# Kernel optimization log

Hardware: AMD Instinct MI355X
Metric: run time of the kernel (lower is better)

## Reference

```python
import jax, jax.numpy as jnp
import numpy as np

B, T, C, H = 256, 256, 384, 64
MAX_REL = 3  # max_relative_position hardcoded in module


def setup_inputs() -> dict:
    key = jax.random.key(0)
    ks = jax.random.split(key, 6)
    s = 1.0 / np.sqrt(C)
    return {
        "x": jax.random.normal(ks[0], (B, T, C), dtype=jnp.float32),
        "Wq": jax.random.normal(ks[1], (C, H), dtype=jnp.float32) * s,
        "Wk": jax.random.normal(ks[2], (C, H), dtype=jnp.float32) * s,
        "Wv": jax.random.normal(ks[3], (C, H), dtype=jnp.float32) * s,
        "rel_k_table": jax.random.normal(ks[4], (2 * MAX_REL + 1, H), dtype=jnp.float32) * s,
        "rel_v_table": jax.random.normal(ks[5], (2 * MAX_REL + 1, H), dtype=jnp.float32) * s,
    }


def reference(x, Wq, Wk, Wv, rel_k_table, rel_v_table):
    Bd, Td, Cd = x.shape
    Hd = Wq.shape[1]
    q = x @ Wq  # [B,T,H]
    k = x @ Wk
    v = x @ Wv
    # relative position indices, clipped Shaw-style
    r = jnp.arange(Td)
    idx = jnp.clip(r[None, :] - r[:, None], -MAX_REL, MAX_REL) + MAX_REL  # [T,T]
    rk = rel_k_table[idx]  # [T,T,H]
    rv = rel_v_table[idx]  # [T,T,H]
    attn1 = jnp.einsum('bth,bsh->bts', q, k)
    attn2 = jnp.einsum('bth,tsh->bts', q, rk)
    scale = jnp.sqrt(jnp.asarray(Hd, dtype=x.dtype))
    scores = (attn1 + attn2) / scale
    causal = jnp.tril(jnp.ones((Td, Td), dtype=bool))
    scores = jnp.where(causal[None, :, :], scores, -jnp.inf)
    attn = jax.nn.softmax(scores, axis=-1)  # dropout = identity (eval mode)
    w1 = jnp.einsum('bts,bsh->bth', attn, v)
    w2 = jnp.einsum('bts,tsh->bth', attn, rv)
    return w1 + w2  # [B,T,H]
```

## Files before the change

### kernel.cpp

```cpp
#include <hip/hip_runtime.h>
#include <hip/hip_bf16.h>


typedef __attribute__((ext_vector_type(8))) __bf16 bf16x8;
typedef __attribute__((ext_vector_type(8))) short short8;
typedef __attribute__((ext_vector_type(4))) float f32x4;
typedef __attribute__((ext_vector_type(4))) int   i32x4;

#define MFMA16(A, B, C) __builtin_amdgcn_mfma_f32_16x16x32_bf16((A), (B), (C), 0, 0, 0)

__device__ __forceinline__ unsigned short f2bf(float f) {
    unsigned int u = __builtin_bit_cast(unsigned int, f);
    u = (u + 0x7FFFu + ((u >> 16) & 1u)) >> 16;
    return (unsigned short)u;
}
__device__ __forceinline__ float bf2f(unsigned short s) {
    unsigned int u = ((unsigned int)s) << 16;
    return __builtin_bit_cast(float, u);
}
__device__ __forceinline__ bf16x8 ld16(const unsigned short* p) {
    return __builtin_bit_cast(bf16x8, *(const i32x4*)p);
}

__global__ void prep_wt(const float* __restrict__ Wq, const float* __restrict__ Wk,
                        const float* __restrict__ Wv, const float* __restrict__ relk,
                        unsigned short* __restrict__ Wt, unsigned short* __restrict__ Rk) {
    int i = blockIdx.x * 256 + threadIdx.x;
    if (i < 3 * 64 * 384) {
        int kk = i % 384;
        int h  = (i / 384) & 63;
        int w  = i / (384 * 64);
        const float* W = (w == 0) ? Wq : ((w == 1) ? Wk : Wv);
        Wt[i] = f2bf(W[kk * 64 + h]);
    } else if (i < 3 * 64 * 384 + 1024) {
        int j = i - 3 * 64 * 384;
        int n = j >> 6, h = j & 63;
        Rk[j] = (n < 4) ? f2bf(relk[n * 64 + h]) : (unsigned short)0;
    }
}

__global__ __launch_bounds__(1024)
__attribute__((amdgpu_waves_per_eu(4, 4)))
void fused_kernel(
        const float* __restrict__ x, const unsigned short* __restrict__ Wt,
        const unsigned short* __restrict__ Rk, const float* __restrict__ relv,
        float* __restrict__ out) {
    extern __shared__ unsigned short sh[];
    unsigned short* ws  = sh;
    unsigned short* ksh = sh;
    unsigned short* vTs = sh + 18432;
    unsigned short* qs  = sh + 35328;
    float* lsum = (float*)(sh + 69120);

    const int tid  = threadIdx.x;
    const int wave = tid >> 6;
    const int lane = tid & 63;
    const int c    = lane & 15;
    const int quad = lane >> 4;
    const int b    = blockIdx.x;

    const f32x4 zero = {0.f, 0.f, 0.f, 0.f};

    const float* xbase = x + (size_t)(b * 256 + wave * 16 + c) * 384 + quad * 8;

    f32x4 aq[4], ak[4], av[4];
#pragma unroll
    for (int nt = 0; nt < 4; nt++) { aq[nt] = zero; ak[nt] = zero; av[nt] = zero; }

    f32x4 tmp[8];
#pragma unroll
    for (int j = 0; j < 4; j++) {
        tmp[2 * j]     = *(const f32x4*)(xbase + j * 32);
        tmp[2 * j + 1] = *(const f32x4*)(xbase + j * 32 + 4);
    }

#pragma unroll
    for (int it = 0; it < 9; it++) {
        int P_ = it * 1024 + tid;
        int r = P_ / 48, pc = P_ % 48;
        i32x4 d = *(const i32x4*)(Wt + r * 384 + pc * 8);
        *(i32x4*)(ws + r * 392 + pc * 8) = d;
    }
    __syncthreads();

#pragma unroll
    for (int ck = 0; ck < 3; ck++) {
        bf16x8 a[4];
#pragma unroll
        for (int j = 0; j < 4; j++) {
            short8 xs8;
#pragma unroll
            for (int e = 0; e < 4; e++) {
                xs8[e]     = (short)f2bf(tmp[2 * j][e]);
                xs8[4 + e] = (short)f2bf(tmp[2 * j + 1][e]);
            }
            a[j] = __builtin_bit_cast(bf16x8, xs8);
        }
        if (ck < 2) {
#pragma unroll
            for (int j = 0; j < 4; j++) {
                const float* xp = xbase + (ck + 1) * 128 + j * 32;
                tmp[2 * j]     = *(const f32x4*)xp;
                tmp[2 * j + 1] = *(const f32x4*)(xp + 4);
            }
        }

#pragma unroll
        for (int j = 0; j < 4; j++) {
            const int col = ck * 128 + j * 32 + quad * 8;
#pragma unroll
            for (int nt = 0; nt < 4; nt++) {
                bf16x8 bq = ld16(ws + (nt * 16 + c) * 392 + col);
                bf16x8 bk = ld16(ws + (64 + nt * 16 + c) * 392 + col);
                bf16x8 aw = ld16(ws + (128 + nt * 16 + c) * 392 + col);
                aq[nt] = MFMA16(a[j], bq, aq[nt]);
                ak[nt] = MFMA16(a[j], bk, ak[nt]);
                av[nt] = MFMA16(aw, a[j], av[nt]);
            }
        }
    }
    __syncthreads();

#pragma unroll
    for (int nt = 0; nt < 4; nt++)
#pragma unroll
        for (int r = 0; r < 4; r++) {
            int row = wave * 16 + quad * 4 + r;
            qs[row * 72 + nt * 16 + c]  = f2bf(aq[nt][r]);
            ksh[row * 72 + nt * 16 + c] = f2bf(ak[nt][r]);
            vTs[(nt * 16 + quad * 4 + r) * 264 + wave * 16 + c] = f2bf(av[nt][r]);
        }
    __syncthreads();

    const int p  = wave & 7;
    const int hi = wave >> 3;
    const int tA = p, tB = 15 - p;

    bf16x8 qA0 = ld16(qs + (tA * 16 + c) * 72 + quad * 8);
    bf16x8 qA1 = ld16(qs + (tA * 16 + c) * 72 + 32 + quad * 8);
    bf16x8 qB0 = ld16(qs + (tB * 16 + c) * 72 + quad * 8);
    bf16x8 qB1 = ld16(qs + (tB * 16 + c) * 72 + 32 + quad * 8);
    float rv[4][2];
#pragma unroll
    for (int j = 0; j < 4; j++)
#pragma unroll
        for (int i = 0; i < 2; i++)
            rv[j][i] = relv[j * 64 + (hi * 2 + i) * 16 + c];
    __syncthreads();

    unsigned short* Pw = sh + 35328 + p * 4224;

#pragma unroll
    for (int it2 = 0; it2 < 2; it2++) {
        const int tt  = it2 ? tB : tA;
        const bf16x8 aq0 = it2 ? qB0 : qA0;
        const bf16x8 aq1 = it2 ? qB1 : qA1;
        const int nst = tt + 1;

        f32x4 e = zero;
        e = MFMA16(aq0, ld16(Rk + c * 64 + quad * 8), e);
        e = MFMA16(aq1, ld16(Rk + c * 64 + 32 + quad * 8), e);
        float ef[4][4];
#pragma unroll
        for (int r = 0; r < 4; r++)
#pragma unroll
            for (int n = 0; n < 4; n++)
                ef[r][n] = __shfl(e[r], (lane & 48) + n, 64);

        float l[4] = {0.f, 0.f, 0.f, 0.f};
#pragma unroll
        for (int st = 0; st < 16; st++) {
            if ((st & 1) == hi) {
                if (st < nst) {
                    const unsigned short* kp = ksh + (st * 16 + c) * 72 + quad * 8;
                    f32x4 s = zero;
                    s = MFMA16(aq0, ld16(kp), s);
                    s = MFMA16(aq1, ld16(kp + 32), s);
#pragma unroll
                    for (int r = 0; r < 4; r++) {
                        int tg = tt * 16 + quad * 4 + r;
                        int sg = st * 16 + c;
                        int d  = sg - tg;
                        float ee = (d <= -3) ? ef[r][0] : (d == -2) ? ef[r][1]
                                 : (d == -1) ? ef[r][2] : ef[r][3];
                        float pv = (d > 0) ? 0.f : __expf(0.125f * (s[r] + ee));
                        l[r] += pv;
                        Pw[(quad * 4 + r) * 264 + sg] = f2bf(pv);
                    }
                } else if (st == nst && (nst & 1)) {
#pragma unroll
                    for (int r = 0; r < 4; r++)
                        Pw[(quad * 4 + r) * 264 + st * 16 + c] = 0;
                }
            }
        }
#pragma unroll
        for (int r = 0; r < 4; r++)
#pragma unroll
            for (int ofs = 1; ofs < 16; ofs <<= 1)
                l[r] += __shfl_xor(l[r], ofs, 64);
        if (c == 0) {
#pragma unroll
            for (int r = 0; r < 4; r++)
                lsum[(p * 2 + hi) * 16 + quad * 4 + r] = l[r];
        }
        __syncthreads();
        float rl[4];
#pragma unroll
        for (int r = 0; r < 4; r++)
            rl[r] = 1.0f / (l[r] + lsum[(p * 2 + (1 - hi)) * 16 + quad * 4 + r]);

        f32x4 o0[2], o1[2];
        o0[0] = zero; o0[1] = zero; o1[0] = zero; o1[1] = zero;
        const int ksteps = (nst + 1) >> 1;
#pragma unroll
        for (int ks = 0; ks < 8; ks++) {
            if (ks < ksteps) {
                bf16x8 ap = ld16(Pw + c * 264 + ks * 32 + quad * 8);
#pragma unroll
                for (int i = 0; i < 2; i++) {
                    const int nt = hi * 2 + i;
                    bf16x8 bv = ld16(vTs + (nt * 16 + c) * 264 + ks * 32 + quad * 8);
                    if (ks & 1) o1[i] = MFMA16(ap, bv, o1[i]);
                    else        o0[i] = MFMA16(ap, bv, o0[i]);
                }
            }
        }

#pragma unroll
        for (int r = 0; r < 4; r++) {
            int tl = quad * 4 + r;
            int tg = tt * 16 + tl;
            float pa  = (tg >= 2) ? bf2f(Pw[tl * 264 + tg - 2]) * rl[r] : 0.f;
            float pb  = (tg >= 1) ? bf2f(Pw[tl * 264 + tg - 1]) * rl[r] : 0.f;
            float pcv = bf2f(Pw[tl * 264 + tg]) * rl[r];
#pragma unroll
            for (int i = 0; i < 2; i++) {
                const int nt = hi * 2 + i;
                float r0 = rv[0][i];
                float w2 = r0 + pa * (rv[1][i] - r0) + pb * (rv[2][i] - r0)
                              + pcv * (rv[3][i] - r0);
                out[(size_t)(b * 256 + tg) * 64 + nt * 16 + c]
                    = (o0[i][r] + o1[i][r]) * rl[r] + w2;
            }
        }
        __syncthreads();
    }
}

extern "C" void kernel_launch(void* const* d_in, const int* in_sizes, int n_in,
                              void* d_out, int out_size, void* d_ws, size_t ws_size,
                              hipStream_t stream) {
    const float* x    = (const float*)d_in[0];
    const float* Wq   = (const float*)d_in[1];
    const float* Wk   = (const float*)d_in[2];
    const float* Wv   = (const float*)d_in[3];
    const float* relk = (const float*)d_in[4];
    const float* relv = (const float*)d_in[5];
    float* out = (float*)d_out;

    char* ws = (char*)d_ws;
    unsigned short* Wt = (unsigned short*)(ws);
    unsigned short* Rk = (unsigned short*)(ws + 147456);

    (void)hipFuncSetAttribute((const void*)fused_kernel,
                              hipFuncAttributeMaxDynamicSharedMemorySize, 150528);

    prep_wt<<<292, 256, 0, stream>>>(Wq, Wk, Wv, relk, Wt, Rk);
    fused_kernel<<<256, 1024, 150528, stream>>>(x, Wt, Rk, relv, out);
}
```

Before: 194.4 us.

## Fold weight transpose/bf16 prep into fused kernel and add MFMA priority hints

Removes the separate prep_wt launch. Each block now loads the fp32 Wq/Wk/Wv and rel_k tables itself, converts them to bf16 and writes them transposed into shared memory, which saves one kernel launch and the round-trip through the workspace. In exchange every block redoes the conversion, reading twice the bytes (fp32 instead of bf16) and doing scattered 2-byte LDS stores. It also wraps the MFMA loops in s_setprio hints to favour the matrix-issuing waves.

```diff
diff --git a/kernel.cpp b/kernel.cpp
--- a/kernel.cpp
+++ b/kernel.cpp
@@ -22,35 +22,20 @@
     return __builtin_bit_cast(bf16x8, *(const i32x4*)p);
 }
 
-__global__ void prep_wt(const float* __restrict__ Wq, const float* __restrict__ Wk,
-                        const float* __restrict__ Wv, const float* __restrict__ relk,
-                        unsigned short* __restrict__ Wt, unsigned short* __restrict__ Rk) {
-    int i = blockIdx.x * 256 + threadIdx.x;
-    if (i < 3 * 64 * 384) {
-        int kk = i % 384;
-        int h  = (i / 384) & 63;
-        int w  = i / (384 * 64);
-        const float* W = (w == 0) ? Wq : ((w == 1) ? Wk : Wv);
-        Wt[i] = f2bf(W[kk * 64 + h]);
-    } else if (i < 3 * 64 * 384 + 1024) {
-        int j = i - 3 * 64 * 384;
-        int n = j >> 6, h = j & 63;
-        Rk[j] = (n < 4) ? f2bf(relk[n * 64 + h]) : (unsigned short)0;
-    }
-}
-
 __global__ __launch_bounds__(1024)
 __attribute__((amdgpu_waves_per_eu(4, 4)))
 void fused_kernel(
-        const float* __restrict__ x, const unsigned short* __restrict__ Wt,
-        const unsigned short* __restrict__ Rk, const float* __restrict__ relv,
-        float* __restrict__ out) {
+        const float* __restrict__ x,
+        const float* __restrict__ Wq, const float* __restrict__ Wk,
+        const float* __restrict__ Wv, const float* __restrict__ relk,
+        const float* __restrict__ relv, float* __restrict__ out) {
     extern __shared__ unsigned short sh[];
     unsigned short* ws  = sh;
     unsigned short* ksh = sh;
     unsigned short* vTs = sh + 18432;
     unsigned short* qs  = sh + 35328;
-    float* lsum = (float*)(sh + 69120);
+    float* lsum = (float*)(sh + 75264);
+    unsigned short* Rkl = sh + 75776;
 
     const int tid  = threadIdx.x;
     const int wave = tid >> 6;
@@ -74,12 +59,23 @@
         tmp[2 * j + 1] = *(const f32x4*)(xbase + j * 32 + 4);
     }
 
-#pragma unroll
-    for (int it = 0; it < 9; it++) {
-        int P_ = it * 1024 + tid;
-        int r = P_ / 48, pc = P_ % 48;
-        i32x4 d = *(const i32x4*)(Wt + r * 384 + pc * 8);
-        *(i32x4*)(ws + r * 392 + pc * 8) = d;
+    {
+        int n = tid >> 6, h = tid & 63;
+        Rkl[n * 72 + h] = (n < 4) ? f2bf(relk[n * 64 + h]) : (unsigned short)0;
+    }
+
+#pragma unroll
+    for (int it = 0; it < 18; it++) {
+        int P_  = it * 1024 + tid;
+        int w   = P_ / 6144;
+        int rem = P_ - w * 6144;
+        int k   = rem >> 4;
+        int h4  = (rem & 15) * 4;
+        const float* Wp = (w == 0) ? Wq : ((w == 1) ? Wk : Wv);
+        f32x4 d = *(const f32x4*)(Wp + k * 64 + h4);
+#pragma unroll
+        for (int e = 0; e < 4; e++)
+            ws[(w * 64 + h4 + e) * 392 + k] = f2bf(d[e]);
     }
     __syncthreads();
 
@@ -105,6 +101,7 @@
             }
         }
 
+        __builtin_amdgcn_s_setprio(1);
 #pragma unroll
         for (int j = 0; j < 4; j++) {
             const int col = ck * 128 + j * 32 + quad * 8;
@@ -118,6 +115,7 @@
                 av[nt] = MFMA16(aw, a[j], av[nt]);
             }
         }
+        __builtin_amdgcn_s_setprio(0);
     }
     __syncthreads();
 
@@ -158,8 +156,8 @@
         const int nst = tt + 1;
 
         f32x4 e = zero;
-        e = MFMA16(aq0, ld16(Rk + c * 64 + quad * 8), e);
-        e = MFMA16(aq1, ld16(Rk + c * 64 + 32 + quad * 8), e);
+        e = MFMA16(aq0, ld16(Rkl + c * 72 + quad * 8), e);
+        e = MFMA16(aq1, ld16(Rkl + c * 72 + 32 + quad * 8), e);
         float ef[4][4];
 #pragma unroll
         for (int r = 0; r < 4; r++)
@@ -213,6 +211,7 @@
         f32x4 o0[2], o1[2];
         o0[0] = zero; o0[1] = zero; o1[0] = zero; o1[1] = zero;
         const int ksteps = (nst + 1) >> 1;
+        __builtin_amdgcn_s_setprio(1);
 #pragma unroll
         for (int ks = 0; ks < 8; ks++) {
             if (ks < ksteps) {
@@ -226,6 +225,7 @@
                 }
             }
         }
+        __builtin_amdgcn_s_setprio(0);
 
 #pragma unroll
         for (int r = 0; r < 4; r++) {
@@ -258,14 +258,10 @@
     const float* relk = (const float*)d_in[4];
     const float* relv = (const float*)d_in[5];
     float* out = (float*)d_out;
-
-    char* ws = (char*)d_ws;
-    unsigned short* Wt = (unsigned short*)(ws);
-    unsigned short* Rk = (unsigned short*)(ws + 147456);
+    (void)d_ws; (void)ws_size; (void)in_sizes; (void)n_in; (void)out_size;
 
     (void)hipFuncSetAttribute((const void*)fused_kernel,
-                              hipFuncAttributeMaxDynamicSharedMemorySize, 150528);
-
-    prep_wt<<<292, 256, 0, stream>>>(Wq, Wk, Wv, relk, Wt, Rk);
-    fused_kernel<<<256, 1024, 150528, stream>>>(x, Wt, Rk, relv, out);
-}
+                              hipFuncAttributeMaxDynamicSharedMemorySize, 153856);
+
+    fused_kernel<<<256, 1024, 153856, stream>>>(x, Wq, Wk, Wv, relk, relv, out);
+}
```

New measurement: 205.8 us. 1.06x slower.
